# Kernel optimization log

Measured on AMD Instinct MI355X. Metric: run time of the kernel, lower is better.

Reference implementation:

```python
import jax, jax.numpy as jnp
import numpy as np

N = 100000
E = 1600000
C_IN = 128
C_OUT = 128
BN_EPS = 1e-5


def setup_inputs() -> dict:
    key = jax.random.key(0)
    k1, k2, k3, k4 = jax.random.split(key, 4)
    x = jax.random.normal(k1, (N, C_IN), dtype=jnp.float32)
    edge_index = jax.random.randint(k2, (2, E), 0, N, dtype=jnp.int64)
    edge_weight = jax.random.uniform(k3, (E,), dtype=jnp.float32)
    W = jax.random.normal(k4, (C_IN, C_OUT), dtype=jnp.float32) / np.sqrt(C_IN)
    gamma = jnp.ones((C_OUT,), dtype=jnp.float32)
    beta = jnp.zeros((C_OUT,), dtype=jnp.float32)
    return {"x": x, "edge_index": edge_index, "edge_weight": edge_weight,
            "W": W, "gamma": gamma, "beta": beta}


def reference(x, edge_index, edge_weight, W, gamma, beta):
    n = x.shape[0]
    row, col = edge_index[0], edge_index[1]  # messages flow row -> col
    loop = jnp.arange(n, dtype=edge_index.dtype)
    # GCNConv (improved=False): add self-loops with weight 1
    row_f = jnp.concatenate([row, loop])
    col_f = jnp.concatenate([col, loop])
    w_f = jnp.concatenate([edge_weight, jnp.ones((n,), x.dtype)])
    # symmetric normalization: D^{-1/2} A D^{-1/2}
    deg = jax.ops.segment_sum(w_f, col_f, num_segments=n)
    deg_safe = jnp.where(deg > 0, deg, 1.0)
    dis = jnp.where(deg > 0, jax.lax.rsqrt(deg_safe), 0.0)
    norm = dis[row_f] * w_f * dis[col_f]  # [E+N]
    # linear transform then scatter-add aggregation (bias=False)
    h = x @ W  # [N, C_out]
    agg = jax.ops.segment_sum(h[row_f] * norm[:, None], col_f, num_segments=n)
    # BatchNorm1d (training mode: batch stats, biased variance) + ReLU
    mean = agg.mean(axis=0)
    var = agg.var(axis=0)
    y = (agg - mean) * jax.lax.rsqrt(var + BN_EPS) * gamma + beta
    return jax.nn.relu(y)
```

## Files before the change

kernel.cpp:

```cpp
#include <hip/hip_runtime.h>

#define C 128
#define MAXNB 1024
typedef unsigned int uint;
typedef unsigned short ushort;
typedef __attribute__((ext_vector_type(4))) float f32x4;
typedef __attribute__((ext_vector_type(8))) short bf16x8;

__device__ __forceinline__ float blo(uint u) { return __uint_as_float(u << 16); }
__device__ __forceinline__ float bhi(uint u) { return __uint_as_float(u & 0xFFFF0000u); }

__global__ __launch_bounds__(256) void k_hist(const int* __restrict__ col,
                                              int* __restrict__ counts,
                                              int nE, int NB, int NBLK) {
    __shared__ int hist[MAXNB];
    const int t = threadIdx.x, blk = blockIdx.x;
    for (int i = t; i < NB; i += 256) hist[i] = 0;
    __syncthreads();
    const int base = blk * 2048;
    for (int k = 0; k < 8; ++k) {
        int e = base + k * 256 + t;
        if (e < nE) atomicAdd(&hist[col[e] >> 7], 1);
    }
    __syncthreads();
    for (int i = t; i < NB; i += 256) counts[i * NBLK + blk] = hist[i];
}

__global__ __launch_bounds__(256) void k_scan1(int* __restrict__ counts,
                                               int* __restrict__ bsum, int scanN) {
    __shared__ int s[256];
    int t = threadIdx.x;
    int i = blockIdx.x * 256 + t;
    int v = (i < scanN) ? counts[i] : 0;
    s[t] = v;
    __syncthreads();
    for (int d = 1; d < 256; d <<= 1) {
        int a = (t >= d) ? s[t - d] : 0;
        __syncthreads();
        s[t] += a;
        __syncthreads();
    }
    if (i < scanN) counts[i] = s[t] - v;
    if (t == 255) bsum[blockIdx.x] = s[255];
}

__global__ __launch_bounds__(256) void k_scan2(int* __restrict__ bsum, int nb) {
    __shared__ int s[256];
    __shared__ int carry;
    int t = threadIdx.x;
    if (t == 0) carry = 0;
    __syncthreads();
    int nch = (nb + 255) / 256;
    for (int c = 0; c < nch; ++c) {
        int i = c * 256 + t;
        int v = (i < nb) ? bsum[i] : 0;
        s[t] = v;
        __syncthreads();
        for (int d = 1; d < 256; d <<= 1) {
            int a = (t >= d) ? s[t - d] : 0;
            __syncthreads();
            s[t] += a;
            __syncthreads();
        }
        int cb = carry;
        if (i < nb) bsum[i] = s[t] - v + cb;
        int tot = s[255];
        __syncthreads();
        if (t == 0) carry = cb + tot;
        __syncthreads();
    }
}

__global__ __launch_bounds__(256) void k_scan3(int* __restrict__ counts,
                                               const int* __restrict__ bsum,
                                               int* __restrict__ bstart,
                                               int scanN, int NBLK, int NB, int nE) {
    int i = blockIdx.x * 256 + threadIdx.x;
    if (i >= scanN) return;
    int v = counts[i] + bsum[i >> 8];
    counts[i] = v;
    if (i % NBLK == 0) {
        bstart[i / NBLK] = v;
        if (i == 0) bstart[NB] = nE;
    }
}

__global__ __launch_bounds__(256) void k_scatter(const int* __restrict__ ei,
                                                 const float* __restrict__ ew,
                                                 const int* __restrict__ counts,
                                                 int2* __restrict__ ev2,
                                                 int nE, int NB, int NBLK) {
    __shared__ int base_l[MAXNB];
    __shared__ int cnt_l[MAXNB];
    const int t = threadIdx.x, blk = blockIdx.x;
    for (int i = t; i < NB; i += 256) {
        base_l[i] = counts[i * NBLK + blk];
        cnt_l[i] = 0;
    }
    __syncthreads();
    const int base = blk * 2048;
    for (int k = 0; k < 8; ++k) {
        int e = base + k * 256 + t;
        if (e >= nE) continue;
        int c = ei[nE + e];
        int row = ei[e];
        int b = c >> 7;
        int pos = base_l[b] + atomicAdd(&cnt_l[b], 1);
        ev2[pos] = make_int2(((c & 127) << 25) | row, __float_as_int(ew[e]));
    }
}

__global__ __launch_bounds__(256) void k_sortdeg(const int2* __restrict__ ev2,
                                                 const int* __restrict__ bstart,
                                                 int2* __restrict__ evs,
                                                 int* __restrict__ offs,
                                                 float* __restrict__ dis,
                                                 int n, int nE) {
    __shared__ int cnt[128];
    __shared__ float wsum[128];
    __shared__ int cur[128];
    __shared__ int sc[128];
    const int t = threadIdx.x, b = blockIdx.x;
    if (t < 128) { cnt[t] = 0; wsum[t] = 0.f; }
    __syncthreads();
    const int s = bstart[b], e = bstart[b + 1];
    for (int i = s + t; i < e; i += 256) {
        int2 E = ev2[i];
        int cl = (uint)E.x >> 25;
        atomicAdd(&cnt[cl], 1);
        atomicAdd(&wsum[cl], __int_as_float(E.y));
    }
    __syncthreads();
    if (t < 128) sc[t] = cnt[t];
    __syncthreads();
    for (int d = 1; d < 128; d <<= 1) {
        int v = 0;
        if (t < 128 && t >= d) v = sc[t - d];
        __syncthreads();
        if (t < 128) sc[t] += v;
        __syncthreads();
    }
    if (t < 128) {
        int col = (b << 7) + t;
        int base = s + sc[t] - cnt[t];
        cur[t] = base;
        if (col < n) {
            offs[col] = base;
            dis[col] = rsqrtf(1.0f + wsum[t]);
        }
    }
    if (b == 0 && t == 0) offs[n] = nE;
    __syncthreads();
    for (int i = s + t; i < e; i += 256) {
        int2 E = ev2[i];
        int cl = (uint)E.x >> 25;
        int pos = atomicAdd(&cur[cl], 1);
        evs[pos] = make_int2(E.x & 0x1FFFFFF, E.y);
    }
}

__global__ __launch_bounds__(256) void k_cvt(const float4* __restrict__ x4,
                                             const float* __restrict__ dis,
                                             ushort4* __restrict__ xb4, long total4) {
    long i = (long)blockIdx.x * 256 + threadIdx.x;
    if (i >= total4) return;
    float d = dis[i >> 5];
    float4 v = x4[i];
    ushort4 r;
#define RNE(OUT, F)                                                     \
    {                                                                   \
        uint u = __float_as_uint((F) * d);                              \
        OUT = (ushort)((u + 0x7FFFu + ((u >> 16) & 1u)) >> 16);         \
    }
    RNE(r.x, v.x) RNE(r.y, v.y) RNE(r.z, v.z) RNE(r.w, v.w)
#undef RNE
    xb4[i] = r;
}

__global__ __launch_bounds__(256) void k_wcvt(const float* __restrict__ W,
                                              ushort* __restrict__ WbT) {
    int idx = blockIdx.x * 256 + threadIdx.x;
    int k = idx >> 7, o = idx & 127;
    uint u = __float_as_uint(W[idx]);
    WbT[o * 128 + k] = (ushort)((u + 0x7FFFu + ((u >> 16) & 1u)) >> 16);
}

__global__ __launch_bounds__(256) void k_segagg(const ushort* __restrict__ xb,
                                                const int2* __restrict__ ev,
                                                const int* __restrict__ offs,
                                                const float* __restrict__ dis,
                                                float* __restrict__ out, int n) {
    const int lane = threadIdx.x & 15;
    const int sub  = threadIdx.x >> 4;
    const int col  = blockIdx.x * 16 + sub;
    if (col >= n) return;

    uint4 sv = *(const uint4*)(xb + (size_t)col * C + lane * 8);
    float acc[8] = {blo(sv.x), bhi(sv.x), blo(sv.y), bhi(sv.y),
                    blo(sv.z), bhi(sv.z), blo(sv.w), bhi(sv.w)};

    int i = offs[col];
    const int end = offs[col + 1];

#define EDGE(E, V)                                                        \
    {                                                                     \
        float nw = __int_as_float(E.y);                                   \
        acc[0] = fmaf(nw, blo(V.x), acc[0]);                              \
        acc[1] = fmaf(nw, bhi(V.x), acc[1]);                              \
        acc[2] = fmaf(nw, blo(V.y), acc[2]);                              \
        acc[3] = fmaf(nw, bhi(V.y), acc[3]);                              \
        acc[4] = fmaf(nw, blo(V.z), acc[4]);                              \
        acc[5] = fmaf(nw, bhi(V.z), acc[5]);                              \
        acc[6] = fmaf(nw, blo(V.w), acc[6]);                              \
        acc[7] = fmaf(nw, bhi(V.w), acc[7]);                              \
    }

    for (; i + 4 <= end; i += 4) {
        int2 e0 = ev[i], e1 = ev[i + 1], e2 = ev[i + 2], e3 = ev[i + 3];
        uint4 v0 = *(const uint4*)(xb + (size_t)e0.x * C + lane * 8);
        uint4 v1 = *(const uint4*)(xb + (size_t)e1.x * C + lane * 8);
        uint4 v2 = *(const uint4*)(xb + (size_t)e2.x * C + lane * 8);
        uint4 v3 = *(const uint4*)(xb + (size_t)e3.x * C + lane * 8);
        EDGE(e0, v0)
        EDGE(e1, v1)
        EDGE(e2, v2)
        EDGE(e3, v3)
    }
    for (; i < end; ++i) {
        int2 e0 = ev[i];
        uint4 v0 = *(const uint4*)(xb + (size_t)e0.x * C + lane * 8);
        EDGE(e0, v0)
    }
#undef EDGE

    float d = dis[col];
    float4* orow = (float4*)(out + (size_t)col * C) + lane * 2;
    orow[0] = make_float4(d * acc[0], d * acc[1], d * acc[2], d * acc[3]);
    orow[1] = make_float4(d * acc[4], d * acc[5], d * acc[6], d * acc[7]);
}

__global__ __launch_bounds__(256, 4) void k_gemm(float* __restrict__ io,
                                                 const ushort* __restrict__ WbT,
                                                 int n) {
    const int t = threadIdx.x;
    const int lane = t & 63;
    const int wv = t >> 6;
    const int lr = lane & 15;
    const int lk = lane >> 4;
    const long m = (long)blockIdx.x * 64 + wv * 16 + lr;
    const bool inr = m < (long)n;

    bf16x8 b[4];
#pragma unroll
    for (int s = 0; s < 4; ++s) {
        uint4 q0 = make_uint4(0, 0, 0, 0), q1 = q0;
        if (inr) {
            const uint4* p = (const uint4*)(io + (size_t)m * C + s * 32 + lk * 8);
            q0 = p[0];
            q1 = p[1];
        }
        union { uint u[4]; bf16x8 v; } cv;
        cv.u[0] = __builtin_amdgcn_perm(q0.y + 0x8000u, q0.x + 0x8000u, 0x07060302u);
        cv.u[1] = __builtin_amdgcn_perm(q0.w + 0x8000u, q0.z + 0x8000u, 0x07060302u);
        cv.u[2] = __builtin_amdgcn_perm(q1.y + 0x8000u, q1.x + 0x8000u, 0x07060302u);
        cv.u[3] = __builtin_amdgcn_perm(q1.w + 0x8000u, q1.z + 0x8000u, 0x07060302u);
        b[s] = cv.v;
    }

    f32x4 acc[8];
#pragma unroll
    for (int ot = 0; ot < 8; ++ot) acc[ot] = (f32x4){0.f, 0.f, 0.f, 0.f};

#pragma unroll 2
    for (int ot = 0; ot < 8; ++ot) {
        const ushort* wp = WbT + (ot * 16 + lr) * 128 + lk * 8;
        bf16x8 a0 = *(const bf16x8*)(wp);
        bf16x8 a1 = *(const bf16x8*)(wp + 32);
        bf16x8 a2 = *(const bf16x8*)(wp + 64);
        bf16x8 a3 = *(const bf16x8*)(wp + 96);
        acc[ot] = __builtin_amdgcn_mfma_f32_16x16x32_bf16(a0, b[0], acc[ot], 0, 0, 0);
        acc[ot] = __builtin_amdgcn_mfma_f32_16x16x32_bf16(a1, b[1], acc[ot], 0, 0, 0);
        acc[ot] = __builtin_amdgcn_mfma_f32_16x16x32_bf16(a2, b[2], acc[ot], 0, 0, 0);
        acc[ot] = __builtin_amdgcn_mfma_f32_16x16x32_bf16(a3, b[3], acc[ot], 0, 0, 0);
    }

    if (inr) {
        float* orow = io + (size_t)m * C + lk * 4;
#pragma unroll
        for (int ot = 0; ot < 8; ++ot)
            *(float4*)(orow + ot * 16) =
                make_float4(acc[ot][0], acc[ot][1], acc[ot][2], acc[ot][3]);
    }
}

__global__ __launch_bounds__(1024) void k_stats(const float4* __restrict__ o4,
                                                float* __restrict__ part, int n) {
    const int t = threadIdx.x;
    const int cg = t & 31;
    const int rl = t >> 5;
    float4 s = make_float4(0.f, 0.f, 0.f, 0.f);
    float4 q = s;
    for (int r = blockIdx.x * 32 + rl; r < n; r += gridDim.x * 32) {
        float4 v = o4[(size_t)r * 32 + cg];
        s.x += v.x; s.y += v.y; s.z += v.z; s.w += v.w;
        q.x = fmaf(v.x, v.x, q.x); q.y = fmaf(v.y, v.y, q.y);
        q.z = fmaf(v.z, v.z, q.z); q.w = fmaf(v.w, v.w, q.w);
    }
    __shared__ float4 ls[1024];
    __shared__ float4 lq[1024];
    ls[t] = s; lq[t] = q;
    __syncthreads();
    for (int d = 512; d >= 32; d >>= 1) {
        if (t < d) {
            float4 a = ls[t + d], bq = lq[t + d];
            ls[t].x += a.x; ls[t].y += a.y; ls[t].z += a.z; ls[t].w += a.w;
            lq[t].x += bq.x; lq[t].y += bq.y; lq[t].z += bq.z; lq[t].w += bq.w;
        }
        __syncthreads();
    }
    if (t < 32) {
        ((float4*)part)[blockIdx.x * 64 + t] = ls[t];
        ((float4*)part)[blockIdx.x * 64 + 32 + t] = lq[t];
    }
}

__global__ __launch_bounds__(256) void k_finish(const float* __restrict__ part,
                                                float* __restrict__ sums, int nblk) {
    int t = threadIdx.x;
    float s = 0.f;
    for (int b = blockIdx.x; b < nblk; b += gridDim.x) s += part[b * 256 + t];
    atomicAdd(&sums[t], s);
}

__global__ __launch_bounds__(256) void k_apply(float* __restrict__ out,
                                               const float* __restrict__ sums,
                                               const float* __restrict__ gamma,
                                               const float* __restrict__ beta,
                                               int n) {
    size_t idx = (size_t)blockIdx.x * 256 + threadIdx.x;
    size_t total = (size_t)n * 32;
    if (idx >= total) return;
    int cg = (int)(idx & 31);
    int c0 = cg * 4;
    float inv_n = 1.0f / (float)n;
    float4 v = ((const float4*)out)[idx];
    float4 r;
#define BN1(OUT, VIN, J)                                                   \
    {                                                                      \
        float mean = sums[c0 + J] * inv_n;                                 \
        float var  = fmaxf(sums[C + c0 + J] * inv_n - mean * mean, 0.f);   \
        float sc   = rsqrtf(var + 1e-5f) * gamma[c0 + J];                  \
        OUT = fmaxf(fmaf(VIN - mean, sc, beta[c0 + J]), 0.f);              \
    }
    BN1(r.x, v.x, 0)
    BN1(r.y, v.y, 1)
    BN1(r.z, v.z, 2)
    BN1(r.w, v.w, 3)
#undef BN1
    ((float4*)out)[idx] = r;
}

extern "C" void kernel_launch(void* const* d_in, const int* in_sizes, int n_in,
                              void* d_out, int out_size, void* d_ws, size_t ws_size,
                              hipStream_t stream) {
    const float* x     = (const float*)d_in[0];
    const int*   ei    = (const int*)d_in[1];
    const float* ew    = (const float*)d_in[2];
    const float* W     = (const float*)d_in[3];
    const float* gamma = (const float*)d_in[4];
    const float* beta  = (const float*)d_in[5];

    const int n  = in_sizes[0] / C;
    const int nE = in_sizes[2];

    const int NB    = (n + 127) >> 7;
    const int NBLK  = (nE + 2047) / 2048;
    const int scanN = NB * NBLK;
    const int scanB = (scanN + 255) / 256;
    const int SB    = 256;

    float* out = (float*)d_out;
    char* p = (char*)d_ws;
#define ALLOC(TYPE, NAME, BYTES) \
    TYPE NAME = (TYPE)p; p += ((size_t)(BYTES) + 255) & ~(size_t)255;
    ALLOC(int2*,   ev2,    (size_t)nE * 8)
    ALLOC(int2*,   evs,    (size_t)nE * 8)
    ALLOC(ushort*, xb,     (size_t)n * C * 2)
    ALLOC(int*,    counts, (size_t)scanN * 4)
    ALLOC(int*,    bsum,   (size_t)scanB * 4)
    ALLOC(int*,    bstart, (size_t)(NB + 1) * 4)
    ALLOC(float*,  dis,    (size_t)n * 4)
    ALLOC(int*,    offs,   (size_t)(n + 1) * 4)
    ALLOC(ushort*, WbT,    32768)
    ALLOC(float*,  sums,   1024)
    ALLOC(float*,  part,   (size_t)SB * 256 * 4)
#undef ALLOC

    const long total4 = (long)n * 32;

    hipMemsetAsync(sums, 0, 256 * 4, stream);

    k_hist   <<<NBLK, 256, 0, stream>>>(ei + nE, counts, nE, NB, NBLK);
    k_scan1  <<<scanB, 256, 0, stream>>>(counts, bsum, scanN);
    k_scan2  <<<1, 256, 0, stream>>>(bsum, scanB);
    k_scan3  <<<scanB, 256, 0, stream>>>(counts, bsum, bstart, scanN, NBLK, NB, nE);
    k_scatter<<<NBLK, 256, 0, stream>>>(ei, ew, counts, ev2, nE, NB, NBLK);
    k_sortdeg<<<NB, 256, 0, stream>>>(ev2, bstart, evs, offs, dis, n, nE);
    k_wcvt   <<<64, 256, 0, stream>>>(W, WbT);
    k_cvt    <<<(int)((total4 + 255) / 256), 256, 0, stream>>>((const float4*)x, dis, (ushort4*)xb, total4);
    k_segagg <<<(n + 15) / 16, 256, 0, stream>>>(xb, evs, offs, dis, out, n);
    k_gemm   <<<(n + 63) / 64, 256, 0, stream>>>(out, WbT, n);
    k_stats  <<<SB, 1024, 0, stream>>>((const float4*)out, part, n);
    k_finish <<<16, 256, 0, stream>>>(part, sums, SB);
    k_apply  <<<(int)((total4 + 255) / 256), 256, 0, stream>>>(out, sums, gamma, beta, n);
}
```

Baseline: 234.4 us.

## Store aggregation as bf16 and fuse BN statistics into GEMM epilogue

```diff
diff --git a/kernel.cpp b/kernel.cpp
--- a/kernel.cpp
+++ b/kernel.cpp
@@ -9,6 +9,8 @@
 
 __device__ __forceinline__ float blo(uint u) { return __uint_as_float(u << 16); }
 __device__ __forceinline__ float bhi(uint u) { return __uint_as_float(u & 0xFFFF0000u); }
+#define PACKBF(LO, HI) __builtin_amdgcn_perm(__float_as_uint(HI) + 0x8000u, \
+                                             __float_as_uint(LO) + 0x8000u, 0x07060302u)
 
 __global__ __launch_bounds__(256) void k_hist(const int* __restrict__ col,
                                               int* __restrict__ counts,
@@ -189,7 +191,7 @@
                                                 const int2* __restrict__ ev,
                                                 const int* __restrict__ offs,
                                                 const float* __restrict__ dis,
-                                                float* __restrict__ out, int n) {
+                                                ushort* __restrict__ aggb, int n) {
     const int lane = threadIdx.x & 15;
     const int sub  = threadIdx.x >> 4;
     const int col  = blockIdx.x * 16 + sub;
@@ -214,34 +216,41 @@
         acc[6] = fmaf(nw, blo(V.w), acc[6]);                              \
         acc[7] = fmaf(nw, bhi(V.w), acc[7]);                              \
     }
-
-    for (; i + 4 <= end; i += 4) {
-        int2 e0 = ev[i], e1 = ev[i + 1], e2 = ev[i + 2], e3 = ev[i + 3];
-        uint4 v0 = *(const uint4*)(xb + (size_t)e0.x * C + lane * 8);
-        uint4 v1 = *(const uint4*)(xb + (size_t)e1.x * C + lane * 8);
-        uint4 v2 = *(const uint4*)(xb + (size_t)e2.x * C + lane * 8);
-        uint4 v3 = *(const uint4*)(xb + (size_t)e3.x * C + lane * 8);
+#define GATH(K) uint4 v##K = *(const uint4*)(xb + (size_t)e##K.x * C + lane * 8);
+
+    for (; i + 8 <= end; i += 8) {
+        int2 e0 = ev[i],     e1 = ev[i + 1], e2 = ev[i + 2], e3 = ev[i + 3];
+        int2 e4 = ev[i + 4], e5 = ev[i + 5], e6 = ev[i + 6], e7 = ev[i + 7];
+        GATH(0) GATH(1) GATH(2) GATH(3) GATH(4) GATH(5) GATH(6) GATH(7)
+        EDGE(e0, v0) EDGE(e1, v1) EDGE(e2, v2) EDGE(e3, v3)
+        EDGE(e4, v4) EDGE(e5, v5) EDGE(e6, v6) EDGE(e7, v7)
+    }
+    for (; i + 2 <= end; i += 2) {
+        int2 e0 = ev[i], e1 = ev[i + 1];
+        GATH(0) GATH(1)
+        EDGE(e0, v0) EDGE(e1, v1)
+    }
+    if (i < end) {
+        int2 e0 = ev[i];
+        GATH(0)
         EDGE(e0, v0)
-        EDGE(e1, v1)
-        EDGE(e2, v2)
-        EDGE(e3, v3)
-    }
-    for (; i < end; ++i) {
-        int2 e0 = ev[i];
-        uint4 v0 = *(const uint4*)(xb + (size_t)e0.x * C + lane * 8);
-        EDGE(e0, v0)
-    }
+    }
+#undef GATH
 #undef EDGE
 
     float d = dis[col];
-    float4* orow = (float4*)(out + (size_t)col * C) + lane * 2;
-    orow[0] = make_float4(d * acc[0], d * acc[1], d * acc[2], d * acc[3]);
-    orow[1] = make_float4(d * acc[4], d * acc[5], d * acc[6], d * acc[7]);
-}
-
-__global__ __launch_bounds__(256, 4) void k_gemm(float* __restrict__ io,
+    uint4 r;
+    r.x = PACKBF(d * acc[0], d * acc[1]);
+    r.y = PACKBF(d * acc[2], d * acc[3]);
+    r.z = PACKBF(d * acc[4], d * acc[5]);
+    r.w = PACKBF(d * acc[6], d * acc[7]);
+    *(uint4*)(aggb + (size_t)col * C + lane * 8) = r;
+}
+
+__global__ __launch_bounds__(256, 4) void k_gemm(const ushort* __restrict__ aggb,
+                                                 float* __restrict__ out,
                                                  const ushort* __restrict__ WbT,
-                                                 int n) {
+                                                 float* __restrict__ part, int n) {
     const int t = threadIdx.x;
     const int lane = t & 63;
     const int wv = t >> 6;
@@ -250,21 +259,15 @@
     const long m = (long)blockIdx.x * 64 + wv * 16 + lr;
     const bool inr = m < (long)n;
 
-    bf16x8 b[4];
-#pragma unroll
-    for (int s = 0; s < 4; ++s) {
-        uint4 q0 = make_uint4(0, 0, 0, 0), q1 = q0;
-        if (inr) {
-            const uint4* p = (const uint4*)(io + (size_t)m * C + s * 32 + lk * 8);
-            q0 = p[0];
-            q1 = p[1];
-        }
-        union { uint u[4]; bf16x8 v; } cv;
-        cv.u[0] = __builtin_amdgcn_perm(q0.y + 0x8000u, q0.x + 0x8000u, 0x07060302u);
-        cv.u[1] = __builtin_amdgcn_perm(q0.w + 0x8000u, q0.z + 0x8000u, 0x07060302u);
-        cv.u[2] = __builtin_amdgcn_perm(q1.y + 0x8000u, q1.x + 0x8000u, 0x07060302u);
-        cv.u[3] = __builtin_amdgcn_perm(q1.w + 0x8000u, q1.z + 0x8000u, 0x07060302u);
-        b[s] = cv.v;
+    bf16x8 b0, b1, b2, b3;
+    if (inr) {
+        const bf16x8* p = (const bf16x8*)(aggb + (size_t)m * C + lk * 8);
+        b0 = p[0];
+        b1 = p[4];
+        b2 = p[8];
+        b3 = p[12];
+    } else {
+        b0 = b1 = b2 = b3 = (bf16x8){0, 0, 0, 0, 0, 0, 0, 0};
     }
 
     f32x4 acc[8];
@@ -278,57 +281,53 @@
         bf16x8 a1 = *(const bf16x8*)(wp + 32);
         bf16x8 a2 = *(const bf16x8*)(wp + 64);
         bf16x8 a3 = *(const bf16x8*)(wp + 96);
-        acc[ot] = __builtin_amdgcn_mfma_f32_16x16x32_bf16(a0, b[0], acc[ot], 0, 0, 0);
-        acc[ot] = __builtin_amdgcn_mfma_f32_16x16x32_bf16(a1, b[1], acc[ot], 0, 0, 0);
-        acc[ot] = __builtin_amdgcn_mfma_f32_16x16x32_bf16(a2, b[2], acc[ot], 0, 0, 0);
-        acc[ot] = __builtin_amdgcn_mfma_f32_16x16x32_bf16(a3, b[3], acc[ot], 0, 0, 0);
-    }
-
-    if (inr) {
-        float* orow = io + (size_t)m * C + lk * 4;
+        acc[ot] = __builtin_amdgcn_mfma_f32_16x16x32_bf16(a0, b0, acc[ot], 0, 0, 0);
+        acc[ot] = __builtin_amdgcn_mfma_f32_16x16x32_bf16(a1, b1, acc[ot], 0, 0, 0);
+        acc[ot] = __builtin_amdgcn_mfma_f32_16x16x32_bf16(a2, b2, acc[ot], 0, 0, 0);
+        acc[ot] = __builtin_amdgcn_mfma_f32_16x16x32_bf16(a3, b3, acc[ot], 0, 0, 0);
+    }
+
+    __shared__ float lds_s[4][128];
+    __shared__ float lds_q[4][128];
+    float* orow = out + (size_t)m * C + lk * 4;
 #pragma unroll
-        for (int ot = 0; ot < 8; ++ot)
+    for (int ot = 0; ot < 8; ++ot) {
+        if (inr)
             *(float4*)(orow + ot * 16) =
                 make_float4(acc[ot][0], acc[ot][1], acc[ot][2], acc[ot][3]);
-    }
-}
-
-__global__ __launch_bounds__(1024) void k_stats(const float4* __restrict__ o4,
-                                                float* __restrict__ part, int n) {
-    const int t = threadIdx.x;
-    const int cg = t & 31;
-    const int rl = t >> 5;
-    float4 s = make_float4(0.f, 0.f, 0.f, 0.f);
-    float4 q = s;
-    for (int r = blockIdx.x * 32 + rl; r < n; r += gridDim.x * 32) {
-        float4 v = o4[(size_t)r * 32 + cg];
-        s.x += v.x; s.y += v.y; s.z += v.z; s.w += v.w;
-        q.x = fmaf(v.x, v.x, q.x); q.y = fmaf(v.y, v.y, q.y);
-        q.z = fmaf(v.z, v.z, q.z); q.w = fmaf(v.w, v.w, q.w);
-    }
-    __shared__ float4 ls[1024];
-    __shared__ float4 lq[1024];
-    ls[t] = s; lq[t] = q;
-    __syncthreads();
-    for (int d = 512; d >= 32; d >>= 1) {
-        if (t < d) {
-            float4 a = ls[t + d], bq = lq[t + d];
-            ls[t].x += a.x; ls[t].y += a.y; ls[t].z += a.z; ls[t].w += a.w;
-            lq[t].x += bq.x; lq[t].y += bq.y; lq[t].z += bq.z; lq[t].w += bq.w;
+        float s0 = acc[ot][0], s1 = acc[ot][1], s2 = acc[ot][2], s3 = acc[ot][3];
+        float q0 = s0 * s0, q1 = s1 * s1, q2 = s2 * s2, q3 = s3 * s3;
+#pragma unroll
+        for (int msk = 1; msk < 16; msk <<= 1) {
+            s0 += __shfl_xor(s0, msk); q0 += __shfl_xor(q0, msk);
+            s1 += __shfl_xor(s1, msk); q1 += __shfl_xor(q1, msk);
+            s2 += __shfl_xor(s2, msk); q2 += __shfl_xor(q2, msk);
+            s3 += __shfl_xor(s3, msk); q3 += __shfl_xor(q3, msk);
         }
-        __syncthreads();
-    }
-    if (t < 32) {
-        ((float4*)part)[blockIdx.x * 64 + t] = ls[t];
-        ((float4*)part)[blockIdx.x * 64 + 32 + t] = lq[t];
-    }
+        if (lr == 0) {
+            int ch = ot * 16 + lk * 4;
+            lds_s[wv][ch + 0] = s0; lds_q[wv][ch + 0] = q0;
+            lds_s[wv][ch + 1] = s1; lds_q[wv][ch + 1] = q1;
+            lds_s[wv][ch + 2] = s2; lds_q[wv][ch + 2] = q2;
+            lds_s[wv][ch + 3] = s3; lds_q[wv][ch + 3] = q3;
+        }
+    }
+    __syncthreads();
+    float ps;
+    if (t < 128)
+        ps = lds_s[0][t] + lds_s[1][t] + lds_s[2][t] + lds_s[3][t];
+    else {
+        int c = t - 128;
+        ps = lds_q[0][c] + lds_q[1][c] + lds_q[2][c] + lds_q[3][c];
+    }
+    part[(size_t)blockIdx.x * 256 + t] = ps;
 }
 
 __global__ __launch_bounds__(256) void k_finish(const float* __restrict__ part,
                                                 float* __restrict__ sums, int nblk) {
     int t = threadIdx.x;
     float s = 0.f;
-    for (int b = blockIdx.x; b < nblk; b += gridDim.x) s += part[b * 256 + t];
+    for (int b = blockIdx.x; b < nblk; b += gridDim.x) s += part[(size_t)b * 256 + t];
     atomicAdd(&sums[t], s);
 }
 
@@ -377,7 +376,7 @@
     const int NBLK  = (nE + 2047) / 2048;
     const int scanN = NB * NBLK;
     const int scanB = (scanN + 255) / 256;
-    const int SB    = 256;
+    const int gB    = (n + 63) / 64;
 
     float* out = (float*)d_out;
     char* p = (char*)d_ws;
@@ -386,6 +385,7 @@
     ALLOC(int2*,   ev2,    (size_t)nE * 8)
     ALLOC(int2*,   evs,    (size_t)nE * 8)
     ALLOC(ushort*, xb,     (size_t)n * C * 2)
+    ALLOC(ushort*, aggb,   (size_t)n * C * 2)
     ALLOC(int*,    counts, (size_t)scanN * 4)
     ALLOC(int*,    bsum,   (size_t)scanB * 4)
     ALLOC(int*,    bstart, (size_t)(NB + 1) * 4)
@@ -393,7 +393,7 @@
     ALLOC(int*,    offs,   (size_t)(n + 1) * 4)
     ALLOC(ushort*, WbT,    32768)
     ALLOC(float*,  sums,   1024)
-    ALLOC(float*,  part,   (size_t)SB * 256 * 4)
+    ALLOC(float*,  part,   (size_t)gB * 256 * 4)
 #undef ALLOC
 
     const long total4 = (long)n * 32;
@@ -408,9 +408,8 @@
     k_sortdeg<<<NB, 256, 0, stream>>>(ev2, bstart, evs, offs, dis, n, nE);
     k_wcvt   <<<64, 256, 0, stream>>>(W, WbT);
     k_cvt    <<<(int)((total4 + 255) / 256), 256, 0, stream>>>((const float4*)x, dis, (ushort4*)xb, total4);
-    k_segagg <<<(n + 15) / 16, 256, 0, stream>>>(xb, evs, offs, dis, out, n);
-    k_gemm   <<<(n + 63) / 64, 256, 0, stream>>>(out, WbT, n);
-    k_stats  <<<SB, 1024, 0, stream>>>((const float4*)out, part, n);
-    k_finish <<<16, 256, 0, stream>>>(part, sums, SB);
+    k_segagg <<<(n + 15) / 16, 256, 0, stream>>>(xb, evs, offs, dis, aggb, n);
+    k_gemm   <<<gB, 256, 0, stream>>>(aggb, out, WbT, part, n);
+    k_finish <<<16, 256, 0, stream>>>(part, sums, gB);
     k_apply  <<<(int)((total4 + 255) / 256), 256, 0, stream>>>(out, sums, gamma, beta, n);
 }
```

Result: slower. 245.8 us (+4.9%).
